# Optimization experiments

Hardware: AMD Instinct MI355X
Metric: run time of the kernel (lower is better)

## Reference

```python
import jax, jax.numpy as jnp
import numpy as np

B, C, L = 4, 512, 4096
H = 8
DH = C // H
MLP = 2048


def _ln(x, g, b, eps=1e-5):
    mu = x.mean(-1, keepdims=True)
    var = ((x - mu) ** 2).mean(-1, keepdims=True)
    return (x - mu) / jnp.sqrt(var + eps) * g + b


def setup_inputs() -> dict:
    key = jax.random.key(0)
    ks = jax.random.split(key, 16)
    s = 0.02
    d = {
        "x": jax.random.normal(ks[0], (B, C, L), jnp.float32),
        "Wq": jax.random.normal(ks[1], (C, C), jnp.float32) * s,
        "bq": jnp.zeros((C,), jnp.float32),
        "gq": jnp.ones((C,), jnp.float32),
        "betaq": jnp.zeros((C,), jnp.float32),
        "Wk": jax.random.normal(ks[2], (C, C), jnp.float32) * s,
        "bk": jnp.zeros((C,), jnp.float32),
        "gk": jnp.ones((C,), jnp.float32),
        "betak": jnp.zeros((C,), jnp.float32),
        "Wv": jax.random.normal(ks[3], (C, C), jnp.float32) * s,
        "bv": jnp.zeros((C,), jnp.float32),
        "gv": jnp.ones((C,), jnp.float32),
        "betav": jnp.zeros((C,), jnp.float32),
        "Wkq": jax.random.normal(ks[4], (C, C), jnp.float32) * s,
        "bkq": jnp.zeros((C,), jnp.float32),
        "Wkk": jax.random.normal(ks[5], (C, C), jnp.float32) * s,
        "bkk": jnp.zeros((C,), jnp.float32),
        "g_attn": jnp.ones((C,), jnp.float32),
        "b_attn": jnp.zeros((C,), jnp.float32),
        "W1": jax.random.normal(ks[6], (C, MLP), jnp.float32) * s,
        "b1": jnp.zeros((MLP,), jnp.float32),
        "W2": jax.random.normal(ks[7], (MLP, C), jnp.float32) * s,
        "b2": jnp.zeros((C,), jnp.float32),
    }
    return d


def _split_heads(t):
    # [B, L, C] -> [B, H, L, DH]
    b, l, _ = t.shape
    return t.reshape(b, l, H, DH).transpose(0, 2, 1, 3)


def reference(x, Wq, bq, gq, betaq, Wk, bk, gk, betak, Wv, bv, gv, betav,
              Wkq, bkq, Wkk, bkk, g_attn, b_attn, W1, b1, W2, b2):
    # x: [B, C, L] -> flatten(2).permute(0,2,1) -> [B, L, C]
    xf = jnp.transpose(x, (0, 2, 1))
    Q = _ln(xf @ Wq + bq, gq, betaq)            # [B, L, C]
    K = _ln(xf @ Wk + bk, gk, betak)            # [B, L, C]
    V = _ln(xf @ Wv + bv, gv, betav)            # [B, L, C]
    # add zero token to K, V (seq dim)
    z = jnp.zeros((x.shape[0], 1, C), x.dtype)
    K = jnp.concatenate([z, K], axis=1)         # [B, Lk, C], Lk = L+1
    V = jnp.concatenate([z, V], axis=1)
    phiQ = jnp.tanh(Q @ Wkq + bkq) + 1.0        # [B, L, C]
    phiK = jnp.tanh(K @ Wkk + bkk) + 1.0        # [B, Lk, C]

    Qh, Kh, Vh = _split_heads(Q), _split_heads(K), _split_heads(V)
    pQ, pK = _split_heads(phiQ), _split_heads(phiK)  # [B,H,L,DH], [B,H,Lk,DH]

    # softmax-reweighted phi_K: score from mean-query probe against K
    q_probe = Qh.mean(axis=2)                                   # [B,H,DH]
    score = jnp.einsum('bhd,bhld->bhl', q_probe, Kh) / jnp.sqrt(jnp.float32(DH))
    score = jax.nn.softmax(score, axis=-1)                      # [B,H,Lk]
    pKw = pK * score[..., None]                                 # [B,H,Lk,DH]

    kv = jnp.einsum('bhld,bhle->bhde', pKw, Vh)                 # [B,H,DH,DH]
    num = jnp.einsum('bhqd,bhde->bhqe', pQ, kv)                 # [B,H,L,DH]
    ksum = pKw.sum(axis=2)                                      # [B,H,DH]
    bottom = jnp.einsum('bhqd,bhd->bhq', pQ, ksum)[..., None] + 1e-6
    out_h = num / bottom                                        # [B,H,L,DH]

    out = out_h.transpose(0, 2, 1, 3).reshape(x.shape[0], -1, C)  # [B,L,C]
    a = _ln(out, g_attn, b_attn)
    m = jax.nn.gelu(a @ W1 + b1, approximate=False) @ W2 + b2
    res = a + m                                                 # residual MLP
    res = jnp.transpose(res, (0, 2, 1))                         # [B,C,L]
    return res + x
```

## Files before the change

kernel.cpp:

```cpp
#include <hip/hip_runtime.h>
#include <math.h>

#define B_ 4
#define C_ 512
#define L_ 4096
#define H_ 8
#define DH_ 64
#define MLP_ 2048
#define BL_ (B_*L_)
#define LK_ (L_+1)

typedef _Float16 f16;
typedef _Float16 f16x8 __attribute__((ext_vector_type(8)));
typedef _Float16 f16x4 __attribute__((ext_vector_type(4)));
typedef float f32x4 __attribute__((ext_vector_type(4)));

__device__ __forceinline__ void gl16(void* lds, const void* g) {
  __builtin_amdgcn_global_load_lds((const __attribute__((address_space(1))) void*)g,
                                   (__attribute__((address_space(3))) void*)lds,
                                   16, 0, 0);
}

__device__ __forceinline__ float frcp(float x) { return __builtin_amdgcn_rcpf(x); }

__global__ __launch_bounds__(256) void transpose_w5(const float* __restrict__ Wq,
                                                    const float* __restrict__ Wk,
                                                    const float* __restrict__ Wv,
                                                    const float* __restrict__ Wkq,
                                                    const float* __restrict__ Wkk,
                                                    f16* __restrict__ dst) {
  int z = blockIdx.z;
  const float* W = (z == 0) ? Wq : (z == 1) ? Wk : (z == 2) ? Wv : (z == 3) ? Wkq : Wkk;
  f16* Wt = dst + (size_t)z * C_ * C_;
  __shared__ float tile[32][33];
  int n0 = blockIdx.x * 32, k0 = blockIdx.y * 32;
  int tx = threadIdx.x & 31, ty = threadIdx.x >> 5;
#pragma unroll
  for (int i = 0; i < 4; ++i)
    tile[ty + i * 8][tx] = W[(size_t)(k0 + ty + i * 8) * C_ + n0 + tx];
  __syncthreads();
#pragma unroll
  for (int i = 0; i < 4; ++i)
    Wt[(size_t)(n0 + ty + i * 8) * C_ + k0 + tx] = (f16)tile[tx][ty + i * 8];
}

__global__ __launch_bounds__(256) void transpose_w12(const float* __restrict__ W1,
                                                     const float* __restrict__ W2,
                                                     f16* __restrict__ W1T,
                                                     f16* __restrict__ W2T) {
  __shared__ float tile[32][33];
  int z = blockIdx.z;
  const float* W = z ? W2 : W1;
  f16* Wt = z ? W2T : W1T;
  int K = z ? MLP_ : C_;
  int N = z ? C_ : MLP_;
  int n0 = (z ? blockIdx.y : blockIdx.x) * 32;
  int k0 = (z ? blockIdx.x : blockIdx.y) * 32;
  int tx = threadIdx.x & 31, ty = threadIdx.x >> 5;
#pragma unroll
  for (int i = 0; i < 4; ++i)
    tile[ty + i * 8][tx] = W[(size_t)(k0 + ty + i * 8) * N + n0 + tx];
  __syncthreads();
#pragma unroll
  for (int i = 0; i < 4; ++i)
    Wt[(size_t)(n0 + ty + i * 8) * K + k0 + tx] = (f16)tile[tx][ty + i * 8];
}

__global__ __launch_bounds__(256) void transpose_x(const float* __restrict__ x,
                                                   f16* __restrict__ xf) {
  __shared__ float tile[32][33];
  int b = blockIdx.z;
  int l0 = blockIdx.x * 32, c0 = blockIdx.y * 32;
  int tx = threadIdx.x & 31, ty = threadIdx.x >> 5;
#pragma unroll
  for (int i = 0; i < 4; ++i)
    tile[ty + i * 8][tx] = x[((size_t)b * C_ + c0 + ty + i * 8) * L_ + l0 + tx];
  __syncthreads();
#pragma unroll
  for (int i = 0; i < 4; ++i)
    xf[((size_t)b * L_ + l0 + ty + i * 8) * C_ + c0 + tx] = (f16)tile[tx][ty + i * 8];
}

__global__ __launch_bounds__(256) void pack_params(
    const float* bq, const float* bk, const float* bv,
    const float* gq, const float* gk, const float* gv,
    const float* betaq, const float* betak, const float* betav,
    const float* bkq, const float* bkk,
    float* bqkv, float* gqkv, float* betaqkv, float* bphi, float* pk0t) {
  int i = blockIdx.x * 256 + threadIdx.x;
  int w = i >> 9, c = i & 511;
  bqkv[i]    = (w == 0 ? bq : (w == 1 ? bk : bv))[c];
  gqkv[i]    = (w == 0 ? gq : (w == 1 ? gk : gv))[c];
  betaqkv[i] = (w == 0 ? betaq : (w == 1 ? betak : betav))[c];
  if (i < 1024) bphi[i] = (i < 512) ? bkq[i] : bkk[i - 512];
  if (i < 512) pk0t[i] = tanhf(bkk[i]) + 1.f;
}

template <int EPI>
__global__ __launch_bounds__(256, 4) void gemm128s(const f16* __restrict__ A,
                                                   const f16* __restrict__ Bt,
                                                   const float* __restrict__ bias,
                                                   f16* __restrict__ Ch,
                                                   int N, int K,
                                                   long long zA, long long zB,
                                                   long long zC, long long zBias) {
  __shared__ f16 smem[16384];
  A  += (size_t)blockIdx.z * zA;
  Bt += (size_t)blockIdx.z * zB;
  Ch += (size_t)blockIdx.z * zC;
  bias += (size_t)blockIdx.z * zBias;

  const int tid = threadIdx.x;
  const int lane = tid & 63, wv = tid >> 6;
  const int wm = wv >> 1, wn = wv & 1;
  const int bm = blockIdx.y * 128, bn = blockIdx.x * 128;
  const int l15 = lane & 15, q = lane >> 4;

  const int srow = tid >> 3;
  const int schunk = (tid & 7) ^ (srow & 7);
  const f16* pa = A + (size_t)(bm + srow) * K + schunk * 8;
  const f16* pb = Bt + (size_t)(bn + srow) * K + schunk * 8;
  f16* la = smem + tid * 8;
  f16* lb = smem + 8192 + tid * 8;
  const int sw0 = (q ^ (lane & 7)) * 8;
  const int sw1 = ((4 + q) ^ (lane & 7)) * 8;

  f32x4 acc[4][4] = {};

  for (int k0 = 0; k0 < K; k0 += 64) {
    __syncthreads();
#pragma unroll
    for (int p = 0; p < 4; ++p) gl16(la + p * 2048, pa + (size_t)p * 32 * K + k0);
#pragma unroll
    for (int p = 0; p < 4; ++p) gl16(lb + p * 2048, pb + (size_t)p * 32 * K + k0);
    __syncthreads();
#pragma unroll
    for (int ks = 0; ks < 2; ++ks) {
      const int sw = ks ? sw1 : sw0;
      f16x8 af[4], bf[4];
#pragma unroll
      for (int i = 0; i < 4; ++i)
        af[i] = *(const f16x8*)&smem[(wm * 64 + i * 16 + l15) * 64 + sw];
#pragma unroll
      for (int j = 0; j < 4; ++j)
        bf[j] = *(const f16x8*)&smem[8192 + (wn * 64 + j * 16 + l15) * 64 + sw];
#pragma unroll
      for (int i = 0; i < 4; ++i)
#pragma unroll
        for (int j = 0; j < 4; ++j)
          acc[i][j] = __builtin_amdgcn_mfma_f32_16x16x32_f16(af[i], bf[j], acc[i][j], 0, 0, 0);
    }
  }

  __syncthreads();
#pragma unroll
  for (int j = 0; j < 4; ++j) {
    int lc = wn * 64 + j * 16 + l15;
    float bb = bias[bn + lc];
#pragma unroll
    for (int i = 0; i < 4; ++i) {
#pragma unroll
      for (int r = 0; r < 4; ++r) {
        int lr = wm * 64 + i * 16 + q * 4 + r;
        float v = acc[i][j][r] + bb;
        if (EPI == 1) {
          v = 2.0f * frcp(1.0f + __expf(-2.0f * v));
        } else if (EPI == 2) {
          v = v * frcp(1.0f + __expf(-1.5957691f * (v + 0.044715f * v * v * v)));
        }
        smem[lr * 128 + ((((lc >> 3) ^ (lr & 15)) << 3) | (lc & 7))] = (f16)v;
      }
    }
  }
  __syncthreads();
#pragma unroll
  for (int p = 0; p < 8; ++p) {
    int idx = p * 256 + tid;
    int row = idx >> 4, ch = idx & 15;
    f16x8 vv = *(const f16x8*)&smem[row * 128 + ((ch ^ (row & 15)) << 3)];
    *(f16x8*)&Ch[(size_t)(bm + row) * N + bn + ch * 8] = vv;
  }
}

template <int EPI>
__global__ __launch_bounds__(512, 2) void gemm256(const f16* __restrict__ A,
                                                  const f16* __restrict__ Bt,
                                                  const float* __restrict__ bias,
                                                  f16* __restrict__ Ch,
                                                  int N, int K,
                                                  long long zA, long long zB,
                                                  long long zC, long long zBias) {
  __shared__ f16 smem[65536];
  A  += (size_t)blockIdx.z * zA;
  Bt += (size_t)blockIdx.z * zB;
  Ch += (size_t)blockIdx.z * zC;
  bias += (size_t)blockIdx.z * zBias;

  const int tid = threadIdx.x;
  const int lane = tid & 63, wv = tid >> 6;
  const int wm = wv >> 2, wn = wv & 3;
  const int bm = blockIdx.x * 256, bn = blockIdx.y * 256;
  const int l15 = lane & 15, q = lane >> 4;

  const int srow = tid >> 3;
  const int schunk = (tid & 7) ^ (srow & 7);
  const f16* pa = A + (size_t)(bm + srow) * K + schunk * 8;
  const f16* pb = Bt + (size_t)(bn + srow) * K + schunk * 8;
  const int sw0 = (q ^ (lane & 7)) * 8;
  const int sw1 = ((4 + q) ^ (lane & 7)) * 8;
  const int NT = K >> 6;

  auto STAGE = [&](int t) {
    f16* bs = smem + (t & 1) * 32768;
    const f16* pat = pa + t * 64;
    const f16* pbt = pb + t * 64;
#pragma unroll
    for (int p = 0; p < 4; ++p) gl16(bs + p * 4096 + tid * 8, pat + (size_t)p * 64 * K);
#pragma unroll
    for (int p = 0; p < 4; ++p) gl16(bs + 16384 + p * 4096 + tid * 8, pbt + (size_t)p * 64 * K);
  };

  f32x4 acc[8][4] = {};

  STAGE(0);
  STAGE(1);

  for (int t = 0; t < NT; ++t) {
    if (t < NT - 1) asm volatile("s_waitcnt vmcnt(8)" ::: "memory");
    else            asm volatile("s_waitcnt vmcnt(0)" ::: "memory");
    __builtin_amdgcn_s_barrier();
    asm volatile("" ::: "memory");

    const f16* As = smem + (t & 1) * 32768;
    const f16* Bs = As + 16384;

    f16x8 bfr[4][2], afr[4][2];
#pragma unroll
    for (int n = 0; n < 4; ++n) {
      bfr[n][0] = *(const f16x8*)&Bs[(wn * 64 + n * 16 + l15) * 64 + sw0];
      bfr[n][1] = *(const f16x8*)&Bs[(wn * 64 + n * 16 + l15) * 64 + sw1];
    }
#pragma unroll
    for (int m = 0; m < 4; ++m) {
      afr[m][0] = *(const f16x8*)&As[(wm * 128 + m * 16 + l15) * 64 + sw0];
      afr[m][1] = *(const f16x8*)&As[(wm * 128 + m * 16 + l15) * 64 + sw1];
    }
    __builtin_amdgcn_s_setprio(1);
#pragma unroll
    for (int ks = 0; ks < 2; ++ks)
#pragma unroll
      for (int m = 0; m < 4; ++m)
#pragma unroll
        for (int n = 0; n < 4; ++n)
          acc[m][n] = __builtin_amdgcn_mfma_f32_16x16x32_f16(afr[m][ks], bfr[n][ks], acc[m][n], 0, 0, 0);
    __builtin_amdgcn_s_setprio(0);
#pragma unroll
    for (int m = 0; m < 4; ++m) {
      afr[m][0] = *(const f16x8*)&As[(wm * 128 + (m + 4) * 16 + l15) * 64 + sw0];
      afr[m][1] = *(const f16x8*)&As[(wm * 128 + (m + 4) * 16 + l15) * 64 + sw1];
    }
    asm volatile("s_waitcnt lgkmcnt(0)" ::: "memory");
    __builtin_amdgcn_s_barrier();
    asm volatile("" ::: "memory");
    if (t + 2 < NT) STAGE(t + 2);
    __builtin_amdgcn_s_setprio(1);
#pragma unroll
    for (int ks = 0; ks < 2; ++ks)
#pragma unroll
      for (int m = 0; m < 4; ++m)
#pragma unroll
        for (int n = 0; n < 4; ++n)
          acc[m + 4][n] = __builtin_amdgcn_mfma_f32_16x16x32_f16(afr[m][ks], bfr[n][ks], acc[m + 4][n], 0, 0, 0);
    __builtin_amdgcn_s_setprio(0);
  }

  __syncthreads();
#pragma unroll
  for (int n = 0; n < 4; ++n) {
    int lc = wn * 64 + n * 16 + l15;
    float bb = bias[bn + lc];
#pragma unroll
    for (int m = 0; m < 8; ++m) {
#pragma unroll
      for (int r = 0; r < 4; ++r) {
        int lr = wm * 128 + m * 16 + q * 4 + r;
        float v = acc[m][n][r] + bb;
        if (EPI == 1) {
          v = 2.0f * frcp(1.0f + __expf(-2.0f * v));
        } else if (EPI == 2) {
          v = v * frcp(1.0f + __expf(-1.5957691f * (v + 0.044715f * v * v * v)));
        }
        smem[lr * 256 + ((((lc >> 3) ^ (lr & 31)) << 3) | (lc & 7))] = (f16)v;
      }
    }
  }
  __syncthreads();
#pragma unroll
  for (int p = 0; p < 16; ++p) {
    int idx = p * 512 + tid;
    int row = idx >> 5, ch = idx & 31;
    f16x8 vv = *(const f16x8*)&smem[row * 256 + ((ch ^ (row & 31)) << 3)];
    *(f16x8*)&Ch[(size_t)(bm + row) * N + bn + ch * 8] = vv;
  }
}

__global__ __launch_bounds__(512, 2) void gemm512d6(const f16* __restrict__ A,
                                                    const f16* __restrict__ Bt,
                                                    const float* __restrict__ bias,
                                                    int N, int K,
                                                    const f16* __restrict__ Ares,
                                                    const float* __restrict__ Xres,
                                                    float* __restrict__ Fout) {
  __shared__ f16 smem[2 * 128 * 128];
  const int tid = threadIdx.x;
  const int lane = tid & 63, wv = tid >> 6;
  const int wm = wv >> 2, wn = wv & 3;
  const int bm = blockIdx.x * 128, bn = blockIdx.y * 128;
  const int l15 = lane & 15, q = lane >> 4;

  const int srow = tid >> 3;
  const int schunk = (tid & 7) ^ (srow & 7);
  const f16* pa = A + (size_t)(bm + srow) * K + schunk * 8;
  const f16* pb = Bt + (size_t)(bn + srow) * K + schunk * 8;
  f16* la = smem + tid * 8;
  f16* lb = smem + 8192 + tid * 8;
  const int sw0 = (q ^ (lane & 7)) * 8;
  const int sw1 = ((4 + q) ^ (lane & 7)) * 8;

  f32x4 acc[4][2] = {};

#pragma unroll
  for (int p = 0; p < 2; ++p) gl16(la + p * 4096, pa + (size_t)p * 64 * K);
#pragma unroll
  for (int p = 0; p < 2; ++p) gl16(lb + p * 4096, pb + (size_t)p * 64 * K);

  int cur = 0;
  for (int k0 = 0; k0 < K; k0 += 64) {
    __syncthreads();
    const int nxt = cur ^ 1;
    if (k0 + 64 < K) {
#pragma unroll
      for (int p = 0; p < 2; ++p) gl16(la + nxt * 16384 + p * 4096, pa + (size_t)p * 64 * K + k0 + 64);
#pragma unroll
      for (int p = 0; p < 2; ++p) gl16(lb + nxt * 16384 + p * 4096, pb + (size_t)p * 64 * K + k0 + 64);
    }
    const f16* As = smem + cur * 16384;
    const f16* Bs = As + 8192;
#pragma unroll
    for (int ks = 0; ks < 2; ++ks) {
      const int sw = ks ? sw1 : sw0;
      f16x8 af[4], bf[2];
#pragma unroll
      for (int i = 0; i < 4; ++i)
        af[i] = *(const f16x8*)&As[(wm * 64 + i * 16 + l15) * 64 + sw];
#pragma unroll
      for (int j = 0; j < 2; ++j)
        bf[j] = *(const f16x8*)&Bs[(wn * 32 + j * 16 + l15) * 64 + sw];
#pragma unroll
      for (int i = 0; i < 4; ++i)
#pragma unroll
        for (int j = 0; j < 2; ++j)
          acc[i][j] = __builtin_amdgcn_mfma_f32_16x16x32_f16(af[i], bf[j], acc[i][j], 0, 0, 0);
    }
    cur = nxt;
  }

  __syncthreads();
#pragma unroll
  for (int j = 0; j < 2; ++j) {
    int lc = wn * 32 + j * 16 + l15;
    float bb = bias[bn + lc];
#pragma unroll
    for (int i = 0; i < 4; ++i) {
#pragma unroll
      for (int r = 0; r < 4; ++r) {
        int lr = wm * 64 + i * 16 + q * 4 + r;
        float v = acc[i][j][r] + bb;
        smem[lr * 128 + ((((lc >> 3) ^ (lr & 15)) << 3) | (lc & 7))] = (f16)v;
      }
    }
  }
  __syncthreads();
#pragma unroll
  for (int p = 0; p < 4; ++p) {
    int idx = p * 512 + tid;
    int row = idx >> 4, ch = idx & 15;
    f16x8 av = *(const f16x8*)&Ares[(size_t)(bm + row) * C_ + bn + ch * 8];
    f16* sp = &smem[row * 128 + ((ch ^ (row & 15)) << 3)];
    f16x8 sv = *(const f16x8*)sp;
#pragma unroll
    for (int jj = 0; jj < 8; ++jj) sv[jj] = (f16)((float)sv[jj] + (float)av[jj]);
    *(f16x8*)sp = sv;
  }
  __syncthreads();
  int c = tid & 127, lh = tid >> 7;
  int b = bm >> 12, lbase = (bm & 4095) + lh * 32;
  const float* xp = Xres + ((size_t)b * C_ + bn + c) * L_ + lbase;
  float* op = Fout + ((size_t)b * C_ + bn + c) * L_ + lbase;
  int chi = c >> 3, clo = c & 7;
#pragma unroll
  for (int s = 0; s < 8; ++s) {
    int l = lh * 32 + s * 4;
    float4 xv = *(const float4*)(xp + s * 4);
    float4 r;
    r.x = (float)smem[(l + 0) * 128 + (((chi ^ ((l + 0) & 15)) << 3) | clo)] + xv.x;
    r.y = (float)smem[(l + 1) * 128 + (((chi ^ ((l + 1) & 15)) << 3) | clo)] + xv.y;
    r.z = (float)smem[(l + 2) * 128 + (((chi ^ ((l + 2) & 15)) << 3) | clo)] + xv.z;
    r.w = (float)smem[(l + 3) * 128 + (((chi ^ ((l + 3) & 15)) << 3) | clo)] + xv.w;
    *(float4*)(op + s * 4) = r;
  }
}

__global__ __launch_bounds__(256, 2) void kv_mfma(const f16* __restrict__ phiK,
                                                  const f16* __restrict__ Vh,
                                                  const float* __restrict__ score,
                                                  float* __restrict__ kvp,
                                                  float* __restrict__ ksum) {
  __shared__ f16 Pt[4096];
  __shared__ f16 Vt[4096];
  __shared__ float red[16][64];
  const int bh = blockIdx.y, b = bh >> 3, h = bh & 7;
  const int l0 = blockIdx.x * 256;
  const int t = threadIdx.x, lane = t & 63, wv = t >> 6;
  const int wd = wv >> 1, we = wv & 1;
  const int l15 = lane & 15, q = lane >> 4;
  const int sw0 = (q ^ (lane & 7)) * 8;
  const int sw1 = ((4 + q) ^ (lane & 7)) * 8;
  const int lb = (t >> 4) * 4;
  const int c4 = (t & 15) * 4;

  float ksacc[4] = {0.f, 0.f, 0.f, 0.f};
  f32x4 acc[2][2] = {};

  for (int cc = 0; cc < 4; ++cc) {
    __syncthreads();
    f16x4 pk4[4], vv4[4];
    float w4[4];
#pragma unroll
    for (int lp = 0; lp < 4; ++lp) {
      int lg = l0 + cc * 64 + lb + lp;
      size_t grow = ((size_t)b * L_ + lg) * C_ + h * DH_ + c4;
      pk4[lp] = *(const f16x4*)(phiK + grow);
      vv4[lp] = *(const f16x4*)(Vh + grow);
      w4[lp] = score[(size_t)bh * LK_ + 1 + lg];
    }
#pragma unroll
    for (int j = 0; j < 4; ++j) {
      int d = c4 + j;
      f16x4 pw, vw;
#pragma unroll
      for (int lp = 0; lp < 4; ++lp) {
        float wp = w4[lp] * (float)pk4[lp][j];
        ksacc[j] += wp;
        pw[lp] = (f16)wp;
        vw[lp] = vv4[lp][j];
      }
      int addr = d * 64 + ((((lb >> 3) ^ (d & 7)) << 3) | (lb & 7));
      *(f16x4*)&Pt[addr] = pw;
      *(f16x4*)&Vt[addr] = vw;
    }
    __syncthreads();
#pragma unroll
    for (int ks = 0; ks < 2; ++ks) {
      const int sw = ks ? sw1 : sw0;
      f16x8 af[2], bf[2];
#pragma unroll
      for (int i = 0; i < 2; ++i)
        af[i] = *(const f16x8*)&Pt[(wd * 32 + i * 16 + l15) * 64 + sw];
#pragma unroll
      for (int j = 0; j < 2; ++j)
        bf[j] = *(const f16x8*)&Vt[(we * 32 + j * 16 + l15) * 64 + sw];
#pragma unroll
      for (int i = 0; i < 2; ++i)
#pragma unroll
        for (int j = 0; j < 2; ++j)
          acc[i][j] = __builtin_amdgcn_mfma_f32_16x16x32_f16(af[i], bf[j], acc[i][j], 0, 0, 0);
    }
  }

  __syncthreads();
#pragma unroll
  for (int j = 0; j < 4; ++j) red[t >> 4][c4 + j] = ksacc[j];
  __syncthreads();
  if (t < 64) {
    float s = 0.f;
#pragma unroll
    for (int g = 0; g < 16; ++g) s += red[g][t];
    atomicAdd(&ksum[bh * 64 + t], s);
  }

  float* dst = kvp + ((size_t)bh * 16 + blockIdx.x) * 4096;
#pragma unroll
  for (int i = 0; i < 2; ++i)
#pragma unroll
    for (int j = 0; j < 2; ++j) {
      int d = wd * 32 + i * 16 + q * 4;
      int e = we * 32 + j * 16 + l15;
      *(f32x4*)&dst[e * 64 + d] = acc[i][j];
    }
}

__global__ __launch_bounds__(256) void build_kvt(const float* __restrict__ kvp,
                                                 f16* __restrict__ kvt) {
  int i = blockIdx.x * 256 + threadIdx.x;
  int bh = i >> 12;
  const float* p = kvp + ((size_t)bh * 16) * 4096 + (i & 4095);
  float v = 0.f;
#pragma unroll
  for (int pp = 0; pp < 16; ++pp) v += p[pp * 4096];
  kvt[i] = (f16)v;
}

__global__ __launch_bounds__(256, 4) void attn_out(const f16* __restrict__ phiQ,
                                                   const f16* __restrict__ kvt,
                                                   const float* __restrict__ ksum,
                                                   const float* __restrict__ score,
                                                   const float* __restrict__ pk0t,
                                                   f16* __restrict__ Ch) {
  __shared__ f16 smem[12288];
  __shared__ float bots[128];
  const int tid = threadIdx.x;
  const int lane = tid & 63, wv = tid >> 6;
  const int bm = blockIdx.x * 128;
  const int h = blockIdx.y;
  const int b = bm >> 12;
  const int l15 = lane & 15, q = lane >> 4;

  const int srow = tid >> 3;
  const int schunk = (tid & 7) ^ (srow & 7);
  const f16* pa = phiQ + (size_t)(bm + srow) * C_ + h * DH_ + schunk * 8;
  const f16* pb = kvt + ((size_t)(b * H_ + h) * DH_ + srow) * DH_ + schunk * 8;
  f16* la = smem + tid * 8;
  f16* lb = smem + 8192 + tid * 8;
  const int sw0 = (q ^ (lane & 7)) * 8;
  const int sw1 = ((4 + q) ^ (lane & 7)) * 8;

#pragma unroll
  for (int p = 0; p < 4; ++p) gl16(la + p * 2048, pa + (size_t)p * 32 * C_);
#pragma unroll
  for (int p = 0; p < 2; ++p) gl16(lb + p * 2048, pb + (size_t)p * 32 * DH_);
  __syncthreads();

  {
    int row = tid >> 1, hf = tid & 1;
    float s0 = score[(size_t)(b * H_ + h) * LK_];
    const float* ksh = ksum + ((size_t)(b * H_ + h)) * 64 + hf * 32;
    const float* pkh = pk0t + h * DH_ + hf * 32;
    float bsum = 0.f;
#pragma unroll
    for (int cc = 0; cc < 4; ++cc) {
      int ch = hf * 4 + cc;
      f16x8 vv2 = *(const f16x8*)&smem[row * 64 + ((ch ^ (row & 7)) << 3)];
#pragma unroll
      for (int j = 0; j < 8; ++j)
        bsum += (float)vv2[j] * (ksh[cc * 8 + j] + s0 * pkh[cc * 8 + j]);
    }
    bsum += __shfl_xor(bsum, 1);
    if (hf == 0) bots[row] = bsum;
  }

  f32x4 acc[2][4] = {};
#pragma unroll
  for (int ks = 0; ks < 2; ++ks) {
    const int sw = ks ? sw1 : sw0;
    f16x8 af[2], bf[4];
#pragma unroll
    for (int i = 0; i < 2; ++i)
      af[i] = *(const f16x8*)&smem[(wv * 32 + i * 16 + l15) * 64 + sw];
#pragma unroll
    for (int j = 0; j < 4; ++j)
      bf[j] = *(const f16x8*)&smem[8192 + (j * 16 + l15) * 64 + sw];
#pragma unroll
    for (int i = 0; i < 2; ++i)
#pragma unroll
      for (int j = 0; j < 4; ++j)
        acc[i][j] = __builtin_amdgcn_mfma_f32_16x16x32_f16(af[i], bf[j], acc[i][j], 0, 0, 0);
  }
  __syncthreads();

#pragma unroll
  for (int j = 0; j < 4; ++j) {
    int lc = j * 16 + l15;
#pragma unroll
    for (int i = 0; i < 2; ++i) {
#pragma unroll
      for (int r = 0; r < 4; ++r) {
        int lr = wv * 32 + i * 16 + q * 4 + r;
        float v = acc[i][j][r] * frcp(bots[lr] + 1e-6f);
        smem[lr * 64 + ((((lc >> 3) ^ (lr & 7)) << 3) | (lc & 7))] = (f16)v;
      }
    }
  }
  __syncthreads();

#pragma unroll
  for (int p = 0; p < 4; ++p) {
    int idx = p * 256 + tid;
    int row = idx >> 3, ch = idx & 7;
    f16x8 vv = *(const f16x8*)&smem[row * 64 + ((ch ^ (row & 7)) << 3)];
    *(f16x8*)&Ch[(size_t)(bm + row) * C_ + h * DH_ + ch * 8] = vv;
  }
}

__global__ __launch_bounds__(256) void ln16(const f16* __restrict__ X,
                                            const float* __restrict__ g,
                                            const float* __restrict__ bta,
                                            f16* __restrict__ Y, int threeway) {
  int wv = threadIdx.x >> 6, lane = threadIdx.x & 63;
  int r = blockIdx.x * 4 + wv;
  int token = r, which = 0;
  if (threeway) { token = r / 3; which = r - token * 3; }
  const f16* xr = X + (size_t)r * C_;
  f16x8 v = *(const f16x8*)(xr + lane * 8);
  float vals[8];
  float s = 0.f, s2 = 0.f;
#pragma unroll
  for (int j = 0; j < 8; ++j) { vals[j] = (float)v[j]; s += vals[j]; s2 += vals[j] * vals[j]; }
#pragma unroll
  for (int m_ = 1; m_ < 64; m_ <<= 1) { s += __shfl_xor(s, m_); s2 += __shfl_xor(s2, m_); }
  float mu = s * (1.f / C_);
  float var = s2 * (1.f / C_) - mu * mu;
  float rstd = rsqrtf(var + 1e-5f);
  const float* gp = g + which * C_;
  const float* bp = bta + which * C_;
  f16x8 o;
#pragma unroll
  for (int j = 0; j < 8; ++j) {
    int c = lane * 8 + j;
    o[j] = (f16)((vals[j] - mu) * rstd * gp[c] + bp[c]);
  }
  *(f16x8*)(Y + ((size_t)which * BL_ + token) * C_ + lane * 8) = o;
}

__global__ __launch_bounds__(256) void qprobe2(const f16* __restrict__ Q,
                                               float* __restrict__ qp) {
  int blk = blockIdx.x;
  int b = blk >> 6;
  int r0 = blk * 64;
  int t = threadIdx.x;
  int c8 = (t & 63) * 8, rg = t >> 6;
  float s[8] = {0.f, 0.f, 0.f, 0.f, 0.f, 0.f, 0.f, 0.f};
#pragma unroll
  for (int i = 0; i < 16; ++i) {
    const f16* row = Q + ((size_t)r0 + rg + i * 4) * C_ + c8;
    f16x8 v = *(const f16x8*)row;
#pragma unroll
    for (int j = 0; j < 8; ++j) s[j] += (float)v[j];
  }
  __shared__ float red[4][520];
#pragma unroll
  for (int j = 0; j < 8; ++j) red[rg][c8 + j] = s[j];
  __syncthreads();
  int c = t * 2;
  float a0 = red[0][c] + red[1][c] + red[2][c] + red[3][c];
  float a1 = red[0][c + 1] + red[1][c + 1] + red[2][c + 1] + red[3][c + 1];
  atomicAdd(&qp[b * C_ + c], a0);
  atomicAdd(&qp[b * C_ + c + 1], a1);
}

__global__ __launch_bounds__(256) void logits_kernel(const f16* __restrict__ Kh,
                                                     const float* __restrict__ qp,
                                                     float* __restrict__ score) {
  int wv = threadIdx.x >> 6, lane = threadIdx.x & 63;
  int token = blockIdx.x * 4 + wv;
  int b = token >> 12;
  int l = token & (L_ - 1);
  const f16* row = Kh + (size_t)token * C_;
  int h = lane >> 3, j0 = (lane & 7) * 8;
  const float* qph = qp + b * C_ + h * DH_ + j0;
  float p = 0.f;
#pragma unroll
  for (int j = 0; j < 8; ++j) p += qph[j] * (float)row[h * DH_ + j0 + j];
  p += __shfl_xor(p, 1); p += __shfl_xor(p, 2); p += __shfl_xor(p, 4);
  if ((lane & 7) == 0)
    score[((size_t)b * H_ + h) * LK_ + 1 + l] = p * (1.f / L_) * 0.125f;
}

__global__ __launch_bounds__(256) void softmax_kernel(float* __restrict__ score) {
  int bh = blockIdx.x, t = threadIdx.x;
  float* s = score + (size_t)bh * LK_;
  __shared__ float red[256];
  float mx = 0.f;
  for (int i = t; i < L_; i += 256) mx = fmaxf(mx, s[1 + i]);
  red[t] = mx; __syncthreads();
  for (int k = 128; k; k >>= 1) { if (t < k) red[t] = fmaxf(red[t], red[t + k]); __syncthreads(); }
  mx = red[0]; __syncthreads();
  float sum = (t == 0) ? expf(-mx) : 0.f;
  for (int i = t; i < L_; i += 256) { float e = expf(s[1 + i] - mx); s[1 + i] = e; sum += e; }
  red[t] = sum; __syncthreads();
  for (int k = 128; k; k >>= 1) { if (t < k) red[t] += red[t + k]; __syncthreads(); }
  float inv = 1.f / red[0];
  __syncthreads();
  for (int i = t; i < L_; i += 256) s[1 + i] *= inv;
  if (t == 0) s[0] = expf(-mx) * inv;
}

extern "C" void kernel_launch(void* const* d_in, const int* in_sizes, int n_in,
                              void* d_out, int out_size, void* d_ws, size_t ws_size,
                              hipStream_t stream) {
  (void)in_sizes; (void)n_in; (void)out_size; (void)ws_size;
  const float* x     = (const float*)d_in[0];
  const float* Wq    = (const float*)d_in[1];
  const float* bq    = (const float*)d_in[2];
  const float* gq    = (const float*)d_in[3];
  const float* betaq = (const float*)d_in[4];
  const float* Wk    = (const float*)d_in[5];
  const float* bk    = (const float*)d_in[6];
  const float* gk    = (const float*)d_in[7];
  const float* betak = (const float*)d_in[8];
  const float* Wv    = (const float*)d_in[9];
  const float* bv    = (const float*)d_in[10];
  const float* gv    = (const float*)d_in[11];
  const float* betav = (const float*)d_in[12];
  const float* Wkq   = (const float*)d_in[13];
  const float* bkq   = (const float*)d_in[14];
  const float* Wkk   = (const float*)d_in[15];
  const float* bkk   = (const float*)d_in[16];
  const float* g_at  = (const float*)d_in[17];
  const float* b_at  = (const float*)d_in[18];
  const float* W1    = (const float*)d_in[19];
  const float* b1    = (const float*)d_in[20];
  const float* W2    = (const float*)d_in[21];
  const float* b2    = (const float*)d_in[22];
  float* out = (float*)d_out;

  char* ws = (char*)d_ws;
  size_t off = 0;
  auto alloc = [&](size_t bytes) -> void* {
    void* p = ws + off;
    off += (bytes + 255) & ~(size_t)255;
    return p;
  };
  f16* U1    = (f16*)alloc((size_t)BL_ * MLP_ * 2);
  f16* QKVh  = (f16*)alloc((size_t)3 * BL_ * C_ * 2);
  f16* phiQK = (f16*)alloc((size_t)2 * BL_ * C_ * 2);
  f16* xf    = (f16*)alloc((size_t)BL_ * C_ * 2);
  f16* WqkvT = (f16*)alloc((size_t)3 * C_ * C_ * 2);
  f16* WkqT  = (f16*)alloc((size_t)C_ * C_ * 2);
  f16* WkkT  = (f16*)alloc((size_t)C_ * C_ * 2);
  f16* W1T   = (f16*)alloc((size_t)C_ * MLP_ * 2);
  f16* W2T   = (f16*)alloc((size_t)MLP_ * C_ * 2);
  f16* kvt   = (f16*)alloc((size_t)B_ * H_ * DH_ * DH_ * 2);
  float* qp    = (float*)alloc((size_t)B_ * C_ * 4);
  float* ksum  = (float*)alloc((size_t)B_ * H_ * DH_ * 4);
  float* score = (float*)alloc((size_t)B_ * H_ * LK_ * 4);
  float* kvp   = (float*)alloc((size_t)B_ * H_ * 16 * 4096 * 4);
  float* bqkv    = (float*)alloc(1536 * 4);
  float* gqkv    = (float*)alloc(1536 * 4);
  float* betaqkv = (float*)alloc(1536 * 4);
  float* bphi    = (float*)alloc(1024 * 4);
  float* pk0t    = (float*)alloc(512 * 4);

  f16* tmpqkv = U1;
  f16* tmpA   = U1;
  f16* h1     = U1;
  f16* Qh = QKVh;
  f16* Kh = QKVh + (size_t)BL_ * C_;
  f16* Vh = QKVh + (size_t)2 * BL_ * C_;
  f16* ah = QKVh;
  f16* phiQ = phiQK;
  f16* phiK = phiQK + (size_t)BL_ * C_;

  dim3 blk(256);
  dim3 blk512(512);

  pack_params<<<6, blk, 0, stream>>>(bq, bk, bv, gq, gk, gv, betaq, betak, betav,
                                     bkq, bkk, bqkv, gqkv, betaqkv, bphi, pk0t);

  transpose_w5<<<dim3(16, 16, 5), blk, 0, stream>>>(Wq, Wk, Wv, Wkq, Wkk, WqkvT);
  transpose_w12<<<dim3(64, 16, 2), blk, 0, stream>>>(W1, W2, W1T, W2T);

  transpose_x<<<dim3(L_ / 32, C_ / 32, B_), blk, 0, stream>>>(x, xf);

  gemm256<5><<<dim3(BL_ / 256, 1536 / 256), blk512, 0, stream>>>(
      xf, WqkvT, bqkv, tmpqkv, 1536, C_, 0, 0, 0, 0);
  ln16<<<3 * BL_ / 4, blk, 0, stream>>>(tmpqkv, gqkv, betaqkv, QKVh, 1);

  hipMemsetAsync(qp, 0, (size_t)(B_ * C_ + B_ * H_ * DH_) * 4, stream);
  qprobe2<<<BL_ / 64, blk, 0, stream>>>(Qh, qp);

  gemm128s<1><<<dim3(C_ / 128, BL_ / 128, 2), blk, 0, stream>>>(
      Qh, WkqT, bphi, phiQ, C_, C_,
      (long long)BL_ * C_, (long long)C_ * C_, (long long)BL_ * C_, (long long)C_);

  logits_kernel<<<BL_ / 4, blk, 0, stream>>>(Kh, qp, score);
  softmax_kernel<<<B_ * H_, blk, 0, stream>>>(score);

  kv_mfma<<<dim3(16, B_ * H_), blk, 0, stream>>>(phiK, Vh, score, kvp, ksum);
  build_kvt<<<(B_ * H_ * DH_ * DH_) / 256, blk, 0, stream>>>(kvp, kvt);

  attn_out<<<dim3(BL_ / 128, H_), blk, 0, stream>>>(phiQ, kvt, ksum, score, pk0t, tmpA);

  ln16<<<BL_ / 4, blk, 0, stream>>>(tmpA, g_at, b_at, ah, 0);

  gemm128s<2><<<dim3(MLP_ / 128, BL_ / 128), blk, 0, stream>>>(
      ah, W1T, b1, h1, MLP_, C_, 0, 0, 0, 0);
  gemm512d6<<<dim3(BL_ / 128, C_ / 128), blk512, 0, stream>>>(
      h1, W2T, b2, C_, MLP_, ah, x, out);
}
```

Before: 381.8 us.

## Fuse LayerNorm into QKV GEMM and attention-output kernels

Replaces the pipelined 256x256 QKV GEMM plus a separate LayerNorm pass with a GEMM whose 64-row tile covers all 512 output columns of one projection, so LayerNorm runs in the epilogue. Likewise the per-head attention-output kernel and the following LayerNorm are merged into one kernel handling all 8 heads for 64 tokens. This removes the write and re-read of two full-size f16 intermediates. In exchange the new QKV GEMM drops double-buffered async staging (a sync before and after every load), and the attention kernel reads kvt straight from global memory, so compute efficiency may fall.

```diff
diff --git a/kernel.cpp b/kernel.cpp
--- a/kernel.cpp
+++ b/kernel.cpp
@@ -96,6 +96,99 @@
   if (i < 512) pk0t[i] = tanhf(bkk[i]) + 1.f;
 }
 
+__global__ __launch_bounds__(512, 2) void gemmqkv_ln(const f16* __restrict__ A,
+                                                     const f16* __restrict__ Wt,
+                                                     const float* __restrict__ bqkv,
+                                                     const float* __restrict__ gqkv,
+                                                     const float* __restrict__ betaqkv,
+                                                     f16* __restrict__ Y) {
+  __shared__ f16 smem[36864];
+  const int which = blockIdx.y;
+  const f16* Bt = Wt + (size_t)which * C_ * C_;
+  const int tid = threadIdx.x;
+  const int lane = tid & 63, wv = tid >> 6;
+  const int bm = blockIdx.x * 64;
+  const int l15 = lane & 15, q = lane >> 4;
+
+  const int srow = tid >> 3;
+  const int schunk = (tid & 7) ^ (srow & 7);
+  const f16* pa = A + (size_t)(bm + srow) * C_ + schunk * 8;
+  const f16* pb = Bt + (size_t)srow * C_ + schunk * 8;
+  f16* la = smem + tid * 8;
+  f16* lb = smem + 4096 + tid * 8;
+  const int sw0 = (q ^ (lane & 7)) * 8;
+  const int sw1 = ((4 + q) ^ (lane & 7)) * 8;
+
+  f32x4 acc[4][4] = {};
+
+  for (int k0 = 0; k0 < C_; k0 += 64) {
+    __syncthreads();
+    gl16(la, pa + k0);
+#pragma unroll
+    for (int p = 0; p < 8; ++p)
+      gl16(lb + p * 4096, pb + (size_t)p * 64 * C_ + k0);
+    __syncthreads();
+#pragma unroll
+    for (int ks = 0; ks < 2; ++ks) {
+      const int sw = ks ? sw1 : sw0;
+      f16x8 af[4], bf[4];
+#pragma unroll
+      for (int i = 0; i < 4; ++i)
+        af[i] = *(const f16x8*)&smem[(i * 16 + l15) * 64 + sw];
+#pragma unroll
+      for (int j = 0; j < 4; ++j)
+        bf[j] = *(const f16x8*)&smem[4096 + (wv * 64 + j * 16 + l15) * 64 + sw];
+#pragma unroll
+      for (int i = 0; i < 4; ++i)
+#pragma unroll
+        for (int j = 0; j < 4; ++j)
+          acc[i][j] = __builtin_amdgcn_mfma_f32_16x16x32_f16(af[i], bf[j], acc[i][j], 0, 0, 0);
+    }
+  }
+
+  __syncthreads();
+#pragma unroll
+  for (int j = 0; j < 4; ++j) {
+    int lc = wv * 64 + j * 16 + l15;
+    float bb = bqkv[which * C_ + lc];
+#pragma unroll
+    for (int i = 0; i < 4; ++i)
+#pragma unroll
+      for (int r = 0; r < 4; ++r) {
+        int lr = i * 16 + q * 4 + r;
+        smem[lr * 528 + lc] = (f16)(acc[i][j][r] + bb);
+      }
+  }
+  __syncthreads();
+
+  {
+    int r = tid >> 3, g = tid & 7;
+    f16x8 vv[8];
+    float s = 0.f, s2 = 0.f;
+#pragma unroll
+    for (int k = 0; k < 8; ++k) {
+      vv[k] = *(const f16x8*)&smem[r * 528 + (k * 8 + g) * 8];
+#pragma unroll
+      for (int j = 0; j < 8; ++j) { float f = (float)vv[k][j]; s += f; s2 += f * f; }
+    }
+    s += __shfl_xor(s, 1); s += __shfl_xor(s, 2); s += __shfl_xor(s, 4);
+    s2 += __shfl_xor(s2, 1); s2 += __shfl_xor(s2, 2); s2 += __shfl_xor(s2, 4);
+    float mu = s * (1.f / C_);
+    float rstd = rsqrtf(s2 * (1.f / C_) - mu * mu + 1e-5f);
+    const float* gp = gqkv + which * C_;
+    const float* bp = betaqkv + which * C_;
+#pragma unroll
+    for (int k = 0; k < 8; ++k) {
+      int c0 = (k * 8 + g) * 8;
+      f16x8 o;
+#pragma unroll
+      for (int j = 0; j < 8; ++j)
+        o[j] = (f16)(((float)vv[k][j] - mu) * rstd * gp[c0 + j] + bp[c0 + j]);
+      *(f16x8*)&Y[((size_t)which * BL_ + bm + r) * C_ + c0] = o;
+    }
+  }
+}
+
 template <int EPI>
 __global__ __launch_bounds__(256, 4) void gemm128s(const f16* __restrict__ A,
                                                    const f16* __restrict__ Bt,
@@ -178,128 +271,6 @@
     int idx = p * 256 + tid;
     int row = idx >> 4, ch = idx & 15;
     f16x8 vv = *(const f16x8*)&smem[row * 128 + ((ch ^ (row & 15)) << 3)];
-    *(f16x8*)&Ch[(size_t)(bm + row) * N + bn + ch * 8] = vv;
-  }
-}
-
-template <int EPI>
-__global__ __launch_bounds__(512, 2) void gemm256(const f16* __restrict__ A,
-                                                  const f16* __restrict__ Bt,
-                                                  const float* __restrict__ bias,
-                                                  f16* __restrict__ Ch,
-                                                  int N, int K,
-                                                  long long zA, long long zB,
-                                                  long long zC, long long zBias) {
-  __shared__ f16 smem[65536];
-  A  += (size_t)blockIdx.z * zA;
-  Bt += (size_t)blockIdx.z * zB;
-  Ch += (size_t)blockIdx.z * zC;
-  bias += (size_t)blockIdx.z * zBias;
-
-  const int tid = threadIdx.x;
-  const int lane = tid & 63, wv = tid >> 6;
-  const int wm = wv >> 2, wn = wv & 3;
-  const int bm = blockIdx.x * 256, bn = blockIdx.y * 256;
-  const int l15 = lane & 15, q = lane >> 4;
-
-  const int srow = tid >> 3;
-  const int schunk = (tid & 7) ^ (srow & 7);
-  const f16* pa = A + (size_t)(bm + srow) * K + schunk * 8;
-  const f16* pb = Bt + (size_t)(bn + srow) * K + schunk * 8;
-  const int sw0 = (q ^ (lane & 7)) * 8;
-  const int sw1 = ((4 + q) ^ (lane & 7)) * 8;
-  const int NT = K >> 6;
-
-  auto STAGE = [&](int t) {
-    f16* bs = smem + (t & 1) * 32768;
-    const f16* pat = pa + t * 64;
-    const f16* pbt = pb + t * 64;
-#pragma unroll
-    for (int p = 0; p < 4; ++p) gl16(bs + p * 4096 + tid * 8, pat + (size_t)p * 64 * K);
-#pragma unroll
-    for (int p = 0; p < 4; ++p) gl16(bs + 16384 + p * 4096 + tid * 8, pbt + (size_t)p * 64 * K);
-  };
-
-  f32x4 acc[8][4] = {};
-
-  STAGE(0);
-  STAGE(1);
-
-  for (int t = 0; t < NT; ++t) {
-    if (t < NT - 1) asm volatile("s_waitcnt vmcnt(8)" ::: "memory");
-    else            asm volatile("s_waitcnt vmcnt(0)" ::: "memory");
-    __builtin_amdgcn_s_barrier();
-    asm volatile("" ::: "memory");
-
-    const f16* As = smem + (t & 1) * 32768;
-    const f16* Bs = As + 16384;
-
-    f16x8 bfr[4][2], afr[4][2];
-#pragma unroll
-    for (int n = 0; n < 4; ++n) {
-      bfr[n][0] = *(const f16x8*)&Bs[(wn * 64 + n * 16 + l15) * 64 + sw0];
-      bfr[n][1] = *(const f16x8*)&Bs[(wn * 64 + n * 16 + l15) * 64 + sw1];
-    }
-#pragma unroll
-    for (int m = 0; m < 4; ++m) {
-      afr[m][0] = *(const f16x8*)&As[(wm * 128 + m * 16 + l15) * 64 + sw0];
-      afr[m][1] = *(const f16x8*)&As[(wm * 128 + m * 16 + l15) * 64 + sw1];
-    }
-    __builtin_amdgcn_s_setprio(1);
-#pragma unroll
-    for (int ks = 0; ks < 2; ++ks)
-#pragma unroll
-      for (int m = 0; m < 4; ++m)
-#pragma unroll
-        for (int n = 0; n < 4; ++n)
-          acc[m][n] = __builtin_amdgcn_mfma_f32_16x16x32_f16(afr[m][ks], bfr[n][ks], acc[m][n], 0, 0, 0);
-    __builtin_amdgcn_s_setprio(0);
-#pragma unroll
-    for (int m = 0; m < 4; ++m) {
-      afr[m][0] = *(const f16x8*)&As[(wm * 128 + (m + 4) * 16 + l15) * 64 + sw0];
-      afr[m][1] = *(const f16x8*)&As[(wm * 128 + (m + 4) * 16 + l15) * 64 + sw1];
-    }
-    asm volatile("s_waitcnt lgkmcnt(0)" ::: "memory");
-    __builtin_amdgcn_s_barrier();
-    asm volatile("" ::: "memory");
-    if (t + 2 < NT) STAGE(t + 2);
-    __builtin_amdgcn_s_setprio(1);
-#pragma unroll
-    for (int ks = 0; ks < 2; ++ks)
-#pragma unroll
-      for (int m = 0; m < 4; ++m)
-#pragma unroll
-        for (int n = 0; n < 4; ++n)
-          acc[m + 4][n] = __builtin_amdgcn_mfma_f32_16x16x32_f16(afr[m][ks], bfr[n][ks], acc[m + 4][n], 0, 0, 0);
-    __builtin_amdgcn_s_setprio(0);
-  }
-
-  __syncthreads();
-#pragma unroll
-  for (int n = 0; n < 4; ++n) {
-    int lc = wn * 64 + n * 16 + l15;
-    float bb = bias[bn + lc];
-#pragma unroll
-    for (int m = 0; m < 8; ++m) {
-#pragma unroll
-      for (int r = 0; r < 4; ++r) {
-        int lr = wm * 128 + m * 16 + q * 4 + r;
-        float v = acc[m][n][r] + bb;
-        if (EPI == 1) {
-          v = 2.0f * frcp(1.0f + __expf(-2.0f * v));
-        } else if (EPI == 2) {
-          v = v * frcp(1.0f + __expf(-1.5957691f * (v + 0.044715f * v * v * v)));
-        }
-        smem[lr * 256 + ((((lc >> 3) ^ (lr & 31)) << 3) | (lc & 7))] = (f16)v;
-      }
-    }
-  }
-  __syncthreads();
-#pragma unroll
-  for (int p = 0; p < 16; ++p) {
-    int idx = p * 512 + tid;
-    int row = idx >> 5, ch = idx & 31;
-    f16x8 vv = *(const f16x8*)&smem[row * 256 + ((ch ^ (row & 31)) << 3)];
     *(f16x8*)&Ch[(size_t)(bm + row) * N + bn + ch * 8] = vv;
   }
 }
@@ -511,125 +482,119 @@
   kvt[i] = (f16)v;
 }
 
-__global__ __launch_bounds__(256, 4) void attn_out(const f16* __restrict__ phiQ,
-                                                   const f16* __restrict__ kvt,
-                                                   const float* __restrict__ ksum,
-                                                   const float* __restrict__ score,
-                                                   const float* __restrict__ pk0t,
-                                                   f16* __restrict__ Ch) {
-  __shared__ f16 smem[12288];
-  __shared__ float bots[128];
+__global__ __launch_bounds__(256, 2) void attn_ln(const f16* __restrict__ phiQ,
+                                                  const f16* __restrict__ kvt,
+                                                  const float* __restrict__ ksum,
+                                                  const float* __restrict__ score,
+                                                  const float* __restrict__ pk0t,
+                                                  const float* __restrict__ g_at,
+                                                  const float* __restrict__ b_at,
+                                                  f16* __restrict__ Y) {
+  __shared__ f16 smem[33792];
+  __shared__ float bots[512];
   const int tid = threadIdx.x;
   const int lane = tid & 63, wv = tid >> 6;
-  const int bm = blockIdx.x * 128;
-  const int h = blockIdx.y;
+  const int bm = blockIdx.x * 64;
   const int b = bm >> 12;
   const int l15 = lane & 15, q = lane >> 4;
 
-  const int srow = tid >> 3;
-  const int schunk = (tid & 7) ^ (srow & 7);
-  const f16* pa = phiQ + (size_t)(bm + srow) * C_ + h * DH_ + schunk * 8;
-  const f16* pb = kvt + ((size_t)(b * H_ + h) * DH_ + srow) * DH_ + schunk * 8;
-  f16* la = smem + tid * 8;
-  f16* lb = smem + 8192 + tid * 8;
-  const int sw0 = (q ^ (lane & 7)) * 8;
-  const int sw1 = ((4 + q) ^ (lane & 7)) * 8;
-
-#pragma unroll
-  for (int p = 0; p < 4; ++p) gl16(la + p * 2048, pa + (size_t)p * 32 * C_);
-#pragma unroll
-  for (int p = 0; p < 2; ++p) gl16(lb + p * 2048, pb + (size_t)p * 32 * DH_);
+#pragma unroll
+  for (int p = 0; p < 16; ++p) {
+    int slot = p * 256 + tid;
+    int row = slot >> 6, c = slot & 63;
+    int cg = (c & ~7) | ((c ^ row) & 7);
+    gl16(smem + (size_t)slot * 8, phiQ + (size_t)(bm + row) * C_ + cg * 8);
+  }
   __syncthreads();
 
   {
-    int row = tid >> 1, hf = tid & 1;
-    float s0 = score[(size_t)(b * H_ + h) * LK_];
-    const float* ksh = ksum + ((size_t)(b * H_ + h)) * 64 + hf * 32;
-    const float* pkh = pk0t + h * DH_ + hf * 32;
-    float bsum = 0.f;
-#pragma unroll
-    for (int cc = 0; cc < 4; ++cc) {
-      int ch = hf * 4 + cc;
-      f16x8 vv2 = *(const f16x8*)&smem[row * 64 + ((ch ^ (row & 7)) << 3)];
+    int r = tid >> 2, hp2 = (tid & 3) * 2;
+#pragma unroll
+    for (int hh = 0; hh < 2; ++hh) {
+      int h = hp2 + hh;
+      float s0 = score[(size_t)(b * H_ + h) * LK_];
+      const float* ksh = ksum + (size_t)(b * H_ + h) * 64;
+      const float* pkh = pk0t + h * 64;
+      float bsum = 0.f;
+#pragma unroll
+      for (int cc = 0; cc < 8; ++cc) {
+        int c = h * 8 + cc;
+        int slot = (c & ~7) | ((c ^ r) & 7);
+        f16x8 vv2 = *(const f16x8*)&smem[r * 512 + slot * 8];
+#pragma unroll
+        for (int j = 0; j < 8; ++j)
+          bsum += (float)vv2[j] * (ksh[cc * 8 + j] + s0 * pkh[cc * 8 + j]);
+      }
+      bots[r * 8 + h] = bsum;
+    }
+  }
+
+  f32x4 acc[2][4][4] = {};
+#pragma unroll
+  for (int hh = 0; hh < 2; ++hh) {
+    int h = wv * 2 + hh;
+    const f16* kb = kvt + (size_t)(b * H_ + h) * 4096;
+#pragma unroll
+    for (int ks = 0; ks < 2; ++ks) {
+      const int sw = ((ks * 4 + q) ^ (l15 & 7)) * 8;
+      f16x8 af[4], bf[4];
+#pragma unroll
+      for (int i = 0; i < 4; ++i)
+        af[i] = *(const f16x8*)&smem[(i * 16 + l15) * 512 + h * 64 + sw];
+#pragma unroll
+      for (int j = 0; j < 4; ++j)
+        bf[j] = *(const f16x8*)&kb[(j * 16 + l15) * 64 + ks * 32 + q * 8];
+#pragma unroll
+      for (int i = 0; i < 4; ++i)
+#pragma unroll
+        for (int j = 0; j < 4; ++j)
+          acc[hh][i][j] = __builtin_amdgcn_mfma_f32_16x16x32_f16(af[i], bf[j], acc[hh][i][j], 0, 0, 0);
+    }
+  }
+  __syncthreads();
+
+#pragma unroll
+  for (int hh = 0; hh < 2; ++hh) {
+    int h = wv * 2 + hh;
+#pragma unroll
+    for (int j = 0; j < 4; ++j) {
+      int lc = h * 64 + j * 16 + l15;
+#pragma unroll
+      for (int i = 0; i < 4; ++i)
+#pragma unroll
+        for (int r = 0; r < 4; ++r) {
+          int lr = i * 16 + q * 4 + r;
+          float v = acc[hh][i][j][r] * frcp(bots[lr * 8 + h] + 1e-6f);
+          smem[lr * 528 + lc] = (f16)v;
+        }
+    }
+  }
+  __syncthreads();
+
+  {
+    int r = tid >> 2, g = tid & 3;
+    f16x8 vv[16];
+    float s = 0.f, s2 = 0.f;
+#pragma unroll
+    for (int k = 0; k < 16; ++k) {
+      vv[k] = *(const f16x8*)&smem[r * 528 + (k * 4 + g) * 8];
+#pragma unroll
+      for (int j = 0; j < 8; ++j) { float f = (float)vv[k][j]; s += f; s2 += f * f; }
+    }
+    s += __shfl_xor(s, 1); s += __shfl_xor(s, 2);
+    s2 += __shfl_xor(s2, 1); s2 += __shfl_xor(s2, 2);
+    float mu = s * (1.f / C_);
+    float rstd = rsqrtf(s2 * (1.f / C_) - mu * mu + 1e-5f);
+#pragma unroll
+    for (int k = 0; k < 16; ++k) {
+      int c0 = (k * 4 + g) * 8;
+      f16x8 o;
 #pragma unroll
       for (int j = 0; j < 8; ++j)
-        bsum += (float)vv2[j] * (ksh[cc * 8 + j] + s0 * pkh[cc * 8 + j]);
-    }
-    bsum += __shfl_xor(bsum, 1);
-    if (hf == 0) bots[row] = bsum;
-  }
-
-  f32x4 acc[2][4] = {};
-#pragma unroll
-  for (int ks = 0; ks < 2; ++ks) {
-    const int sw = ks ? sw1 : sw0;
-    f16x8 af[2], bf[4];
-#pragma unroll
-    for (int i = 0; i < 2; ++i)
-      af[i] = *(const f16x8*)&smem[(wv * 32 + i * 16 + l15) * 64 + sw];
-#pragma unroll
-    for (int j = 0; j < 4; ++j)
-      bf[j] = *(const f16x8*)&smem[8192 + (j * 16 + l15) * 64 + sw];
-#pragma unroll
-    for (int i = 0; i < 2; ++i)
-#pragma unroll
-      for (int j = 0; j < 4; ++j)
-        acc[i][j] = __builtin_amdgcn_mfma_f32_16x16x32_f16(af[i], bf[j], acc[i][j], 0, 0, 0);
-  }
-  __syncthreads();
-
-#pragma unroll
-  for (int j = 0; j < 4; ++j) {
-    int lc = j * 16 + l15;
-#pragma unroll
-    for (int i = 0; i < 2; ++i) {
-#pragma unroll
-      for (int r = 0; r < 4; ++r) {
-        int lr = wv * 32 + i * 16 + q * 4 + r;
-        float v = acc[i][j][r] * frcp(bots[lr] + 1e-6f);
-        smem[lr * 64 + ((((lc >> 3) ^ (lr & 7)) << 3) | (lc & 7))] = (f16)v;
-      }
-    }
-  }
-  __syncthreads();
-
-#pragma unroll
-  for (int p = 0; p < 4; ++p) {
-    int idx = p * 256 + tid;
-    int row = idx >> 3, ch = idx & 7;
-    f16x8 vv = *(const f16x8*)&smem[row * 64 + ((ch ^ (row & 7)) << 3)];
-    *(f16x8*)&Ch[(size_t)(bm + row) * C_ + h * DH_ + ch * 8] = vv;
-  }
-}
-
-__global__ __launch_bounds__(256) void ln16(const f16* __restrict__ X,
-                                            const float* __restrict__ g,
-                                            const float* __restrict__ bta,
-                                            f16* __restrict__ Y, int threeway) {
-  int wv = threadIdx.x >> 6, lane = threadIdx.x & 63;
-  int r = blockIdx.x * 4 + wv;
-  int token = r, which = 0;
-  if (threeway) { token = r / 3; which = r - token * 3; }
-  const f16* xr = X + (size_t)r * C_;
-  f16x8 v = *(const f16x8*)(xr + lane * 8);
-  float vals[8];
-  float s = 0.f, s2 = 0.f;
-#pragma unroll
-  for (int j = 0; j < 8; ++j) { vals[j] = (float)v[j]; s += vals[j]; s2 += vals[j] * vals[j]; }
-#pragma unroll
-  for (int m_ = 1; m_ < 64; m_ <<= 1) { s += __shfl_xor(s, m_); s2 += __shfl_xor(s2, m_); }
-  float mu = s * (1.f / C_);
-  float var = s2 * (1.f / C_) - mu * mu;
-  float rstd = rsqrtf(var + 1e-5f);
-  const float* gp = g + which * C_;
-  const float* bp = bta + which * C_;
-  f16x8 o;
-#pragma unroll
-  for (int j = 0; j < 8; ++j) {
-    int c = lane * 8 + j;
-    o[j] = (f16)((vals[j] - mu) * rstd * gp[c] + bp[c]);
-  }
-  *(f16x8*)(Y + ((size_t)which * BL_ + token) * C_ + lane * 8) = o;
+        o[j] = (f16)(((float)vv[k][j] - mu) * rstd * g_at[c0 + j] + b_at[c0 + j]);
+      *(f16x8*)&Y[(size_t)(bm + r) * C_ + c0] = o;
+    }
+  }
 }
 
 __global__ __launch_bounds__(256) void qprobe2(const f16* __restrict__ Q,
@@ -751,9 +716,7 @@
   float* bphi    = (float*)alloc(1024 * 4);
   float* pk0t    = (float*)alloc(512 * 4);
 
-  f16* tmpqkv = U1;
-  f16* tmpA   = U1;
-  f16* h1     = U1;
+  f16* h1 = U1;
   f16* Qh = QKVh;
   f16* Kh = QKVh + (size_t)BL_ * C_;
   f16* Vh = QKVh + (size_t)2 * BL_ * C_;
@@ -772,9 +735,8 @@
 
   transpose_x<<<dim3(L_ / 32, C_ / 32, B_), blk, 0, stream>>>(x, xf);
 
-  gemm256<5><<<dim3(BL_ / 256, 1536 / 256), blk512, 0, stream>>>(
-      xf, WqkvT, bqkv, tmpqkv, 1536, C_, 0, 0, 0, 0);
-  ln16<<<3 * BL_ / 4, blk, 0, stream>>>(tmpqkv, gqkv, betaqkv, QKVh, 1);
+  gemmqkv_ln<<<dim3(BL_ / 64, 3), blk512, 0, stream>>>(
+      xf, WqkvT, bqkv, gqkv, betaqkv, QKVh);
 
   hipMemsetAsync(qp, 0, (size_t)(B_ * C_ + B_ * H_ * DH_) * 4, stream);
   qprobe2<<<BL_ / 64, blk, 0, stream>>>(Qh, qp);
@@ -789,9 +751,7 @@
   kv_mfma<<<dim3(16, B_ * H_), blk, 0, stream>>>(phiK, Vh, score, kvp, ksum);
   build_kvt<<<(B_ * H_ * DH_ * DH_) / 256, blk, 0, stream>>>(kvp, kvt);
 
-  attn_out<<<dim3(BL_ / 128, H_), blk, 0, stream>>>(phiQ, kvt, ksum, score, pk0t, tmpA);
-
-  ln16<<<BL_ / 4, blk, 0, stream>>>(tmpA, g_at, b_at, ah, 0);
+  attn_ln<<<BL_ / 64, blk, 0, stream>>>(phiQ, kvt, ksum, score, pk0t, g_at, b_at, ah);
 
   gemm128s<2><<<dim3(MLP_ / 128, BL_ / 128), blk, 0, stream>>>(
       ah, W1T, b1, h1, MLP_, C_, 0, 0, 0, 0);
```

After: 398.3 us. 4.3% more time.
